# Kernel tuning notes

Measured on AMD Instinct MI355X. Metric: run time of the kernel, lower is better.

Reference implementation:

```python
import math
import jax, jax.numpy as jnp
import numpy as np

B = 128          # graphs per batch
N = 1024         # nodes per graph
E = 1048576      # total edges (avg degree 8)
F_IN = 64
NHID = 64
NCLS = 10
RATIO = 0.8


def setup_inputs() -> dict:
    key = jax.random.key(0)
    ks = jax.random.split(key, 24)
    x = jax.random.normal(ks[0], (B * N, F_IN), jnp.float32)
    # intra-graph random edges: graph id per edge, local src/dst
    epg = E // B
    gid = jnp.repeat(jnp.arange(B, dtype=jnp.int32), epg)
    src = gid * N + jax.random.randint(ks[1], (E,), 0, N, jnp.int32)
    dst = gid * N + jax.random.randint(ks[2], (E,), 0, N, jnp.int32)
    def lin(k, fi, fo):
        s = 1.0 / np.sqrt(fi)
        return jax.random.uniform(k, (fi, fo), jnp.float32, -s, s)
    p = {
        'W1': lin(ks[3], F_IN, NHID), 'b1': jnp.zeros((NHID,), jnp.float32),
        'Wp1': lin(ks[4], NHID, 1), 'bp1': jnp.zeros((1,), jnp.float32),
        'W2': lin(ks[5], NHID, NHID), 'b2': jnp.zeros((NHID,), jnp.float32),
        'Wp2': lin(ks[6], NHID, 1), 'bp2': jnp.zeros((1,), jnp.float32),
        'W3': lin(ks[7], NHID, NHID), 'b3': jnp.zeros((NHID,), jnp.float32),
        'Wp3': lin(ks[8], NHID, 1), 'bp3': jnp.zeros((1,), jnp.float32),
        'L1w': lin(ks[9], 2 * NHID, NHID), 'L1b': jnp.zeros((NHID,), jnp.float32),
        'L2w': lin(ks[10], NHID, NHID // 2), 'L2b': jnp.zeros((NHID // 2,), jnp.float32),
        'L3w': lin(ks[11], NHID // 2, NCLS), 'L3b': jnp.zeros((NCLS,), jnp.float32),
    }
    return dict(x=x, edge_src=src, edge_dst=dst, **p)


def gcn_conv(x, W, b, src, dst, emask, n):
    # PyG GCNConv: add self loops, symmetric deg normalization
    xw = x @ W
    ew = emask.astype(x.dtype)
    deg = jax.ops.segment_sum(ew, dst, num_segments=n) + 1.0  # +1 self loop
    dis = jax.lax.rsqrt(deg)
    norm = dis[src] * dis[dst] * ew
    agg = jax.ops.segment_sum(xw[src] * norm[:, None], dst, num_segments=n)
    agg = agg + xw * (dis * dis)[:, None]  # self-loop message
    return agg + b


def sag_pool(x, Wp, bp, src, dst, emask, n_cur):
    n_tot = B * n_cur
    k = int(math.ceil(RATIO * n_cur))
    score = gcn_conv(x, Wp, bp, src, dst, emask, n_tot)[:, 0]
    _, idx = jax.lax.top_k(score.reshape(B, n_cur), k)
    perm = (idx + (jnp.arange(B, dtype=jnp.int32) * n_cur)[:, None]).reshape(-1)
    xn = x[perm] * jnp.tanh(score[perm])[:, None]
    new_idx = jnp.full((n_tot,), -1, jnp.int32).at[perm].set(
        jnp.arange(B * k, dtype=jnp.int32))
    ns, nd = new_idx[src], new_idx[dst]
    valid = emask & (ns >= 0) & (nd >= 0)
    return xn, jnp.where(valid, ns, 0), jnp.where(valid, nd, 0), valid, k


def readout(x, k):
    xr = x.reshape(B, k, NHID)
    return jnp.concatenate([xr.max(axis=1), xr.mean(axis=1)], axis=1)


def reference(x, edge_src, edge_dst, W1, b1, Wp1, bp1, W2, b2, Wp2, bp2,
              W3, b3, Wp3, bp3, L1w, L1b, L2w, L2b, L3w, L3b):
    src = edge_src.astype(jnp.int32)
    dst = edge_dst.astype(jnp.int32)
    emask = jnp.ones((E,), bool)
    n = N
    h = jax.nn.relu(gcn_conv(x, W1, b1, src, dst, emask, B * n))
    h, src, dst, emask, n = sag_pool(h, Wp1, bp1, src, dst, emask, n)
    r1 = readout(h, n)
    h = jax.nn.relu(gcn_conv(h, W2, b2, src, dst, emask, B * n))
    h, src, dst, emask, n = sag_pool(h, Wp2, bp2, src, dst, emask, n)
    r2 = readout(h, n)
    h = jax.nn.relu(gcn_conv(h, W3, b3, src, dst, emask, B * n))
    h, src, dst, emask, n = sag_pool(h, Wp3, bp3, src, dst, emask, n)
    r3 = readout(h, n)
    z = r1 + r2 + r3
    z = jax.nn.relu(z @ L1w + L1b)          # dropout is identity in eval
    z = jax.nn.relu(z @ L2w + L2b)
    return jax.nn.log_softmax(z @ L3w + L3b, axis=-1)
```

## Files before the change

kernel.cpp:

```cpp
#include <hip/hip_runtime.h>
#include <math.h>

constexpr int B_   = 128;
constexpr int N_   = 1024;
constexpr int E_   = 1048576;
constexpr int BN_  = B_ * N_;
constexpr int EPG  = E_ / B_;
constexpr int SRT2 = EPG + 3 * 1024;
constexpr int NSEG = 16;

typedef short v8s __attribute__((ext_vector_type(8)));
typedef float v4f __attribute__((ext_vector_type(4)));

__device__ __forceinline__ unsigned bf16_rne(unsigned u) {
    return (u + 0x7FFFu + ((u >> 16) & 1u)) >> 16;
}

__global__ __launch_bounds__(1024) void k_csr2(
        const int* __restrict__ src, const int* __restrict__ dst,
        const int* __restrict__ cum,
        int* __restrict__ srt, int* __restrict__ rowptr,
        float* __restrict__ dis, int n) {
    __shared__ int cnt[1024];
    __shared__ int cur[1024];
    __shared__ int cums[1024];
    __shared__ int wsum[17];
    int g = blockIdx.x, tid = threadIdx.x;
    int gb   = g * N_;
    int base = g * n;
    const int eb = g * EPG;
    int* gsrt = srt + (size_t)g * SRT2;

    cums[tid] = cum ? cum[gb + tid] : tid;
    cnt[tid] = 0;
    __syncthreads();
    for (int t = tid; t < EPG; t += 1024) {
        int s = cums[src[eb + t] - gb];
        int d = cums[dst[eb + t] - gb];
        if ((s | d) >= 0) atomicAdd(&cnt[d], 1);
    }
    __syncthreads();

    int c  = (tid < n) ? cnt[tid] : 0;
    int pc = (c + 3) & ~3;
    int v = pc;
    int lane = tid & 63, wv = tid >> 6;
    #pragma unroll
    for (int off = 1; off < 64; off <<= 1) {
        int t = __shfl_up(v, off, 64);
        if (lane >= off) v += t;
    }
    if (lane == 63) wsum[wv] = v;
    __syncthreads();
    if (tid == 0) {
        int run = 0;
        #pragma unroll
        for (int i = 0; i < 16; ++i) { int t = wsum[i]; wsum[i] = run; run += t; }
        wsum[16] = run;
    }
    __syncthreads();
    int excl = v - pc + wsum[wv];
    if (tid < n) {
        cur[tid] = excl;
        rowptr[g * (n + 1) + tid] = excl;
        dis[base + tid] = rsqrtf((float)c + 1.0f);
    }
    if (tid == 0) rowptr[g * (n + 1) + n] = wsum[16];
    __syncthreads();

    for (int t = tid; t < EPG; t += 1024) {
        int s = cums[src[eb + t] - gb];
        int d = cums[dst[eb + t] - gb];
        if ((s | d) < 0) continue;
        int pos = atomicAdd(&cur[d], 1);
        gsrt[pos] = s;
    }
    __syncthreads();

    if (tid < n) {
        int e1 = excl + pc;
        for (int t = cur[tid]; t < e1; ++t) gsrt[t] = n;
    }
}

__global__ __launch_bounds__(1024) void k_wprep3(
        const float* __restrict__ W0, const float* __restrict__ W1,
        const float* __restrict__ W2, unsigned short* __restrict__ wfall) {
    const float* W = (blockIdx.x == 0) ? W0 : (blockIdx.x == 1) ? W1 : W2;
    unsigned short* wf = wfall + (size_t)blockIdx.x * 8192;
    int t = threadIdx.x;
    int l  = t & 63;
    int kk = (t >> 6) & 1;
    int c  = (t >> 7) & 3;
    int p  = (t >> 9) & 1;
    int col = c * 16 + (l & 15);
    int kbase = kk * 32 + (l >> 4) * 8;
    unsigned short o[8];
    #pragma unroll
    for (int j = 0; j < 8; ++j) {
        float w = W[(kbase + j) * 64 + col];
        unsigned u  = __float_as_uint(w);
        unsigned hi = bf16_rne(u);
        if (p == 0) o[j] = (unsigned short)hi;
        else {
            float lo = w - __uint_as_float(hi << 16);
            o[j] = (unsigned short)bf16_rne(__float_as_uint(lo));
        }
    }
    uint4 v;
    v.x = o[0] | ((unsigned)o[1] << 16);
    v.y = o[2] | ((unsigned)o[3] << 16);
    v.z = o[4] | ((unsigned)o[5] << 16);
    v.w = o[6] | ((unsigned)o[7] << 16);
    *reinterpret_cast<uint4*>(wf + (size_t)t * 8) = v;
}

__global__ __launch_bounds__(256) void k_xw_mfma(
        const float* __restrict__ h, const int* __restrict__ perm,
        const float* __restrict__ ggate, const unsigned short* __restrict__ wf,
        const float* __restrict__ dis, float* __restrict__ xwq, int rows) {
    __shared__ float hs[128][68];
    __shared__ float sdis[128];
    __shared__ int   lperm[128];
    __shared__ float lgate[128];
    int tid = threadIdx.x;
    int r0 = blockIdx.x * 128;

    if (perm) {
        if (tid < 128) { lperm[tid] = perm[r0 + tid]; lgate[tid] = ggate[r0 + tid]; }
        __syncthreads();
        for (int i = tid; i < 128 * 16; i += 256) {
            int row = i >> 4, s = i & 15;
            float4 v = *reinterpret_cast<const float4*>(h + (size_t)lperm[row] * 64 + s * 4);
            float gt = lgate[row];
            v.x *= gt; v.y *= gt; v.z *= gt; v.w *= gt;
            *reinterpret_cast<float4*>(&hs[row][s * 4]) = v;
        }
    } else {
        for (int i = tid; i < 128 * 16; i += 256) {
            int row = i >> 4, s = i & 15;
            float4 v = *reinterpret_cast<const float4*>(h + (size_t)(r0 + row) * 64 + s * 4);
            *reinterpret_cast<float4*>(&hs[row][s * 4]) = v;
        }
    }
    if (tid < 128) sdis[tid] = dis[r0 + tid];

    int lane = tid & 63;
    v8s wh[4][2], wl[4][2];
    #pragma unroll
    for (int c = 0; c < 4; ++c) {
        #pragma unroll
        for (int kk = 0; kk < 2; ++kk) {
            wh[c][kk] = *reinterpret_cast<const v8s*>(wf + (((size_t)((0*4 + c)*2 + kk))*64 + lane)*8);
            wl[c][kk] = *reinterpret_cast<const v8s*>(wf + (((size_t)((1*4 + c)*2 + kk))*64 + lane)*8);
        }
    }
    __syncthreads();

    int wave = tid >> 6;
    int m = lane & 15, b = lane >> 4;
    #pragma unroll
    for (int t = 0; t < 2; ++t) {
        int lr0 = (wave * 2 + t) * 16;
        float f[16];
        *reinterpret_cast<float4*>(f)      = *reinterpret_cast<const float4*>(&hs[lr0 + m][b * 8]);
        *reinterpret_cast<float4*>(f + 4)  = *reinterpret_cast<const float4*>(&hs[lr0 + m][b * 8 + 4]);
        *reinterpret_cast<float4*>(f + 8)  = *reinterpret_cast<const float4*>(&hs[lr0 + m][32 + b * 8]);
        *reinterpret_cast<float4*>(f + 12) = *reinterpret_cast<const float4*>(&hs[lr0 + m][32 + b * 8 + 4]);
        v8s ah[2], al[2];
        #pragma unroll
        for (int ch = 0; ch < 2; ++ch) {
            #pragma unroll
            for (int j = 0; j < 8; ++j) {
                float x = f[ch * 8 + j];
                unsigned u  = __float_as_uint(x);
                unsigned hi = bf16_rne(u);
                float lo = x - __uint_as_float(hi << 16);
                ah[ch][j] = (short)hi;
                al[ch][j] = (short)bf16_rne(__float_as_uint(lo));
            }
        }
        float dv[4];
        #pragma unroll
        for (int reg = 0; reg < 4; ++reg) dv[reg] = sdis[lr0 + b * 4 + reg];

        #pragma unroll
        for (int c = 0; c < 4; ++c) {
            v4f acc = {0.f, 0.f, 0.f, 0.f};
            acc = __builtin_amdgcn_mfma_f32_16x16x32_bf16(ah[0], wh[c][0], acc, 0, 0, 0);
            acc = __builtin_amdgcn_mfma_f32_16x16x32_bf16(ah[1], wh[c][1], acc, 0, 0, 0);
            acc = __builtin_amdgcn_mfma_f32_16x16x32_bf16(al[0], wh[c][0], acc, 0, 0, 0);
            acc = __builtin_amdgcn_mfma_f32_16x16x32_bf16(al[1], wh[c][1], acc, 0, 0, 0);
            acc = __builtin_amdgcn_mfma_f32_16x16x32_bf16(ah[0], wl[c][0], acc, 0, 0, 0);
            acc = __builtin_amdgcn_mfma_f32_16x16x32_bf16(ah[1], wl[c][1], acc, 0, 0, 0);
            acc = __builtin_amdgcn_mfma_f32_16x16x32_bf16(al[0], wl[c][0], acc, 0, 0, 0);
            acc = __builtin_amdgcn_mfma_f32_16x16x32_bf16(al[1], wl[c][1], acc, 0, 0, 0);
            #pragma unroll
            for (int reg = 0; reg < 4; ++reg) {
                int grow = r0 + lr0 + b * 4 + reg;
                xwq[((size_t)c * rows + grow) * 16 + m] = acc[reg] * dv[reg];
            }
        }
    }
}

__global__ __launch_bounds__(1024, 8) void k_agg8(
        const int* __restrict__ srt, const int* __restrict__ rowptr,
        const float* __restrict__ dis, const float* __restrict__ xwq,
        const float* __restrict__ bias, const float* __restrict__ Wp,
        float* __restrict__ hout, float* __restrict__ sagg8,
        int n, int rows) {
    extern __shared__ float xs[];
    int lrpPad = (n + 4) & ~3;
    int* lrp = (int*)(xs + (n + 1) * 12);
    unsigned short* lsrtU = (unsigned short*)(lrp + lrpPad);

    int g = blockIdx.x & 127, e8 = blockIdx.x >> 7;
    int q = e8 >> 1, half = (e8 & 1) * 8;
    int foff = q * 16 + half;
    int tid  = threadIdx.x;
    int base = g * n;
    const float* plane = xwq + ((size_t)q * rows + base) * 16 + half;

    for (int i = tid; i < n * 2; i += 1024) {
        int row = i >> 1, s = i & 1;
        float4 v = *reinterpret_cast<const float4*>(plane + row * 16 + s * 4);
        *reinterpret_cast<float4*>(xs + row * 12 + s * 4) = v;
    }
    if (tid < 12) xs[n * 12 + tid] = 0.0f;
    for (int i = tid; i <= n; i += 1024) lrp[i] = rowptr[g * (n + 1) + i];
    __syncthreads();
    int total = lrp[n];
    const int* gsrt = srt + (size_t)g * SRT2;
    for (int i = tid; i < total; i += 1024) lsrtU[i] = (unsigned short)gsrt[i];
    __syncthreads();

    int sub = tid & 1;
    float4 bq  = *reinterpret_cast<const float4*>(bias + foff + sub * 4);
    float4 wp4 = *reinterpret_cast<const float4*>(Wp   + foff + sub * 4);
    for (int row = tid >> 1; row < n; row += 512) {
        int s0 = lrp[row], s1 = lrp[row + 1];
        float4 acc = *reinterpret_cast<const float4*>(xs + row * 12 + sub * 4);
        for (int j = s0; j < s1; j += 4) {
            ushort4 nb = *reinterpret_cast<const ushort4*>(lsrtU + j);
            const float4 v0 = *reinterpret_cast<const float4*>(xs + nb.x * 12 + sub * 4);
            const float4 v1 = *reinterpret_cast<const float4*>(xs + nb.y * 12 + sub * 4);
            const float4 v2 = *reinterpret_cast<const float4*>(xs + nb.z * 12 + sub * 4);
            const float4 v3 = *reinterpret_cast<const float4*>(xs + nb.w * 12 + sub * 4);
            acc.x += v0.x + v1.x + v2.x + v3.x;
            acc.y += v0.y + v1.y + v2.y + v3.y;
            acc.z += v0.z + v1.z + v2.z + v3.z;
            acc.w += v0.w + v1.w + v2.w + v3.w;
        }
        float dsc = dis[base + row];
        float4 o;
        o.x = fmaxf(fmaf(dsc, acc.x, bq.x), 0.0f);
        o.y = fmaxf(fmaf(dsc, acc.y, bq.y), 0.0f);
        o.z = fmaxf(fmaf(dsc, acc.z, bq.z), 0.0f);
        o.w = fmaxf(fmaf(dsc, acc.w, bq.w), 0.0f);
        *reinterpret_cast<float4*>(hout + (size_t)(base + row) * 64 + foff + sub * 4) = o;
        float part = o.x * wp4.x + o.y * wp4.y + o.z * wp4.z + o.w * wp4.w;
        part += __shfl_xor(part, 1, 64);
        if (sub == 0) xs[row * 12 + 8] = part * dsc;
    }
    __syncthreads();

    for (int row = tid; row < n; row += 1024) {
        float acc = xs[row * 12 + 8];
        int s1 = lrp[row + 1];
        for (int j = lrp[row]; j < s1; j += 4) {
            ushort4 nb = *reinterpret_cast<const ushort4*>(lsrtU + j);
            acc += xs[nb.x * 12 + 8] + xs[nb.y * 12 + 8]
                 + xs[nb.z * 12 + 8] + xs[nb.w * 12 + 8];
        }
        sagg8[(size_t)e8 * BN_ + base + row] = acc;
    }
}

__global__ __launch_bounds__(1024) void k_score_topk(
        const float* __restrict__ dis, const float* __restrict__ sagg8,
        const float* __restrict__ bp, int n, int k,
        int* __restrict__ perm, float* __restrict__ ggate,
        int* __restrict__ cum, int do_compose) {
    __shared__ unsigned long long keys[1024];
    __shared__ int mark[1024];
    int g = blockIdx.x, tid = threadIdx.x;
    int base = g * n;
    float bp0 = bp[0];

    unsigned long long kv = 0ull;
    if (tid < n) {
        float s0 = 0.0f;
        #pragma unroll
        for (int p = 0; p < 8; ++p) s0 += sagg8[(size_t)p * BN_ + base + tid];
        float sag = dis[base + tid] * s0 + bp0;
        unsigned u  = __float_as_uint(sag);
        unsigned mk = (u & 0x80000000u) ? ~u : (u | 0x80000000u);
        kv = ((unsigned long long)mk << 32) | (unsigned)tid;
    }
    keys[tid] = kv;
    mark[tid] = -1;

    for (int size = 2; size <= 1024; size <<= 1) {
        for (int stride = size >> 1; stride > 0; stride >>= 1) {
            __syncthreads();
            if (tid < 512) {
                int a  = ((tid / stride) * (stride << 1)) + (tid & (stride - 1));
                int bx = a + stride;
                bool asc = ((a & size) == 0);
                unsigned long long ka = keys[a], kb = keys[bx];
                bool sw = asc ? (ka > kb) : (ka < kb);
                if (sw) { keys[a] = kb; keys[bx] = ka; }
            }
        }
    }
    __syncthreads();

    if (tid < k) {
        int j = tid;
        unsigned long long kvv = keys[1023 - j];
        int local   = (int)(kvv & 0xFFFFFFFFull);
        unsigned mk = (unsigned)(kvv >> 32);
        unsigned u  = (mk & 0x80000000u) ? (mk ^ 0x80000000u) : ~mk;
        int newg = g * k + j;
        perm[newg]  = base + local;
        ggate[newg] = tanhf(__uint_as_float(u));
        mark[local] = j;
    }
    __syncthreads();
    if (do_compose) {
        int gb = g * N_;
        int c = (do_compose == 1) ? tid : cum[gb + tid];
        cum[gb + tid] = (c >= 0) ? mark[c] : -1;
    }
}

__global__ __launch_bounds__(256) void k_readout_seg(
        const float* __restrict__ h, const int* __restrict__ perm,
        const float* __restrict__ ggate, int k, float* __restrict__ pz) {
    int g = blockIdx.x / NSEG, seg = blockIdx.x % NSEG;
    int ck = (k + NSEG - 1) / NSEG;
    int j0 = seg * ck;
    int j1 = min(k, j0 + ck);
    __shared__ float gate[64];
    __shared__ int   lperm[64];
    int tid = threadIdx.x;
    for (int j = j0 + tid; j < j1; j += 256) {
        lperm[j - j0] = perm[g * k + j];
        gate[j - j0]  = ggate[g * k + j];
    }
    __syncthreads();
    int lane = tid & 63, w = tid >> 6;
    float mx = -INFINITY, sm = 0.0f;
    for (int j = j0 + w; j < j1; j += 4) {
        float v = h[(size_t)lperm[j - j0] * 64 + lane] * gate[j - j0];
        mx = fmaxf(mx, v); sm += v;
    }
    __shared__ float smx[4][64], ssm[4][64];
    smx[w][lane] = mx; ssm[w][lane] = sm;
    __syncthreads();
    if (w == 0) {
        #pragma unroll
        for (int i = 1; i < 4; ++i) { mx = fmaxf(mx, smx[i][lane]); sm += ssm[i][lane]; }
        float* p = pz + ((size_t)g * NSEG + seg) * 128;
        p[lane]      = mx;
        p[64 + lane] = sm;
    }
}

__global__ __launch_bounds__(128) void k_mlp(const float* __restrict__ pz,
                      const float* __restrict__ L1w, const float* __restrict__ L1b,
                      const float* __restrict__ L2w, const float* __restrict__ L2b,
                      const float* __restrict__ L3w, const float* __restrict__ L3b,
                      float* __restrict__ out) {
    __shared__ float z[128], h1[64], h2[32], lg[10], lse;
    int g = blockIdx.x, tid = threadIdx.x;
    const float kinv[3] = {1.0f / 820.0f, 1.0f / 656.0f, 1.0f / 525.0f};
    float zv = 0.0f;
    if (tid < 64) {
        #pragma unroll
        for (int L = 0; L < 3; ++L) {
            const float* p = pz + (((size_t)L * B_ + g) * NSEG) * 128;
            float mx = -INFINITY;
            #pragma unroll
            for (int s = 0; s < NSEG; ++s) mx = fmaxf(mx, p[s * 128 + tid]);
            zv += mx;
        }
    } else {
        int f = tid - 64;
        #pragma unroll
        for (int L = 0; L < 3; ++L) {
            const float* p = pz + (((size_t)L * B_ + g) * NSEG) * 128;
            float sm = 0.0f;
            #pragma unroll
            for (int s = 0; s < NSEG; ++s) sm += p[s * 128 + 64 + f];
            zv += sm * kinv[L];
        }
    }
    z[tid] = zv;
    __syncthreads();
    if (tid < 64) {
        float acc = L1b[tid];
        for (int i = 0; i < 128; ++i) acc = fmaf(z[i], L1w[i * 64 + tid], acc);
        h1[tid] = fmaxf(acc, 0.0f);
    }
    __syncthreads();
    if (tid < 32) {
        float acc = L2b[tid];
        for (int i = 0; i < 64; ++i) acc = fmaf(h1[i], L2w[i * 32 + tid], acc);
        h2[tid] = fmaxf(acc, 0.0f);
    }
    __syncthreads();
    if (tid < 10) {
        float acc = L3b[tid];
        for (int i = 0; i < 32; ++i) acc = fmaf(h2[i], L3w[i * 10 + tid], acc);
        lg[tid] = acc;
    }
    __syncthreads();
    if (tid == 0) {
        float m = lg[0];
        for (int i = 1; i < 10; ++i) m = fmaxf(m, lg[i]);
        float s = 0.0f;
        for (int i = 0; i < 10; ++i) s += expf(lg[i] - m);
        lse = m + logf(s);
    }
    __syncthreads();
    if (tid < 10) out[g * 10 + tid] = lg[tid] - lse;
}

extern "C" void kernel_launch(void* const* d_in, const int* in_sizes, int n_in,
                              void* d_out, int out_size, void* d_ws, size_t ws_size,
                              hipStream_t stream) {
    const float* x    = (const float*)d_in[0];
    const int*   esrc = (const int*)d_in[1];
    const int*   edst = (const int*)d_in[2];
    const float* W [3] = {(const float*)d_in[3],  (const float*)d_in[7],  (const float*)d_in[11]};
    const float* bb[3] = {(const float*)d_in[4],  (const float*)d_in[8],  (const float*)d_in[12]};
    const float* Wp[3] = {(const float*)d_in[5],  (const float*)d_in[9],  (const float*)d_in[13]};
    const float* bp[3] = {(const float*)d_in[6],  (const float*)d_in[10], (const float*)d_in[14]};
    const float* L1w = (const float*)d_in[15];
    const float* L1b = (const float*)d_in[16];
    const float* L2w = (const float*)d_in[17];
    const float* L2b = (const float*)d_in[18];
    const float* L3w = (const float*)d_in[19];
    const float* L3b = (const float*)d_in[20];
    float* out = (float*)d_out;

    float* fws   = (float*)d_ws;
    float* agg   = fws;
    float* xwq   = agg  + (size_t)BN_ * 64;
    float* dis   = xwq  + (size_t)BN_ * 64;
    float* sagg8 = dis  + BN_;
    float* ggate = sagg8 + 8 * (size_t)BN_;
    float* pz    = ggate + BN_;
    int*   perm   = (int*)(pz + 3 * B_ * NSEG * 128);
    int*   cum    = perm + BN_;
    int*   srt    = cum + BN_;
    int*   rowptr = srt + (size_t)B_ * SRT2;
    unsigned short* wfrag = (unsigned short*)(rowptr + B_ * (N_ + 1));

    hipFuncSetAttribute(reinterpret_cast<const void*>(k_agg8),
                        hipFuncAttributeMaxDynamicSharedMemorySize,
                        1025 * 12 * 4 + 1028 * 4 + SRT2 * 2);

    k_wprep3<<<3, 1024, 0, stream>>>(W[0], W[1], W[2], wfrag);

    const int ks_[3] = {820, 656, 525};
    int n = N_;

    for (int L = 0; L < 3; ++L) {
        int rows = B_ * n;
        int k    = ks_[L];

        k_csr2<<<B_, 1024, 0, stream>>>(esrc, edst, (L == 0) ? nullptr : cum,
                                        srt, rowptr, dis, n);

        if (L == 0)
            k_xw_mfma<<<rows / 128, 256, 0, stream>>>(x, nullptr, nullptr,
                                                      wfrag, dis, xwq, rows);
        else
            k_xw_mfma<<<rows / 128, 256, 0, stream>>>(agg, perm, ggate,
                                                      wfrag + (size_t)L * 8192, dis, xwq, rows);

        int lrpPad = (n + 4) & ~3;
        size_t ldsB = (size_t)(n + 1) * 12 * 4 + (size_t)lrpPad * 4 + (size_t)SRT2 * 2;
        k_agg8<<<B_ * 8, 1024, ldsB, stream>>>(
            srt, rowptr, dis, xwq, bb[L], Wp[L], agg, sagg8, n, rows);

        k_score_topk<<<B_, 1024, 0, stream>>>(dis, sagg8, bp[L], n, k,
                                              perm, ggate, cum, (L < 2) ? (L + 1) : 0);

        k_readout_seg<<<B_ * NSEG, 256, 0, stream>>>(agg, perm, ggate, k,
                                                     pz + (size_t)L * B_ * NSEG * 128);

        n = k;
    }

    k_mlp<<<B_, 128, 0, stream>>>(pz, L1w, L1b, L2w, L2b, L3w, L3b, out);
}
```

Measured before the change: 264.6 us.

## Replace LDS-staged feature-plane aggregation with wave-per-row global gather

Drops the 8-way feature-split aggregation kernel, which staged a graph's feature plane and CSR into LDS. Each wave now owns a run of rows and gathers full 64-wide rows from a row-major xw buffer in global memory, one lane per feature. The CSR no longer pads rows to multiples of 4, and neighbour reduction of the SAG score is moved into the top-k kernel, which works from a single per-node partial score instead of 8 partial planes. This removes the LDS staging and padding work but relies on uncached global gathers with serial per-edge loop latency and fewer, larger blocks.

New measurement: 351.6 us. 1.33x slower.

```diff
diff --git a/kernel.cpp b/kernel.cpp
--- a/kernel.cpp
+++ b/kernel.cpp
@@ -6,7 +6,6 @@
 constexpr int E_   = 1048576;
 constexpr int BN_  = B_ * N_;
 constexpr int EPG  = E_ / B_;
-constexpr int SRT2 = EPG + 3 * 1024;
 constexpr int NSEG = 16;
 
 typedef short v8s __attribute__((ext_vector_type(8)));
@@ -29,7 +28,6 @@
     int gb   = g * N_;
     int base = g * n;
     const int eb = g * EPG;
-    int* gsrt = srt + (size_t)g * SRT2;
 
     cums[tid] = cum ? cum[gb + tid] : tid;
     cnt[tid] = 0;
@@ -41,9 +39,8 @@
     }
     __syncthreads();
 
-    int c  = (tid < n) ? cnt[tid] : 0;
-    int pc = (c + 3) & ~3;
-    int v = pc;
+    int c = (tid < n) ? cnt[tid] : 0;
+    int v = c;
     int lane = tid & 63, wv = tid >> 6;
     #pragma unroll
     for (int off = 1; off < 64; off <<= 1) {
@@ -59,7 +56,7 @@
         wsum[16] = run;
     }
     __syncthreads();
-    int excl = v - pc + wsum[wv];
+    int excl = v - c + wsum[wv];
     if (tid < n) {
         cur[tid] = excl;
         rowptr[g * (n + 1) + tid] = excl;
@@ -73,13 +70,7 @@
         int d = cums[dst[eb + t] - gb];
         if ((s | d) < 0) continue;
         int pos = atomicAdd(&cur[d], 1);
-        gsrt[pos] = s;
-    }
-    __syncthreads();
-
-    if (tid < n) {
-        int e1 = excl + pc;
-        for (int t = cur[tid]; t < e1; ++t) gsrt[t] = n;
+        srt[eb + pos] = s;
     }
 }
 
@@ -118,7 +109,7 @@
 __global__ __launch_bounds__(256) void k_xw_mfma(
         const float* __restrict__ h, const int* __restrict__ perm,
         const float* __restrict__ ggate, const unsigned short* __restrict__ wf,
-        const float* __restrict__ dis, float* __restrict__ xwq, int rows) {
+        const float* __restrict__ dis, float* __restrict__ xw, int rows) {
     __shared__ float hs[128][68];
     __shared__ float sdis[128];
     __shared__ int   lperm[128];
@@ -198,102 +189,72 @@
             #pragma unroll
             for (int reg = 0; reg < 4; ++reg) {
                 int grow = r0 + lr0 + b * 4 + reg;
-                xwq[((size_t)c * rows + grow) * 16 + m] = acc[reg] * dv[reg];
+                xw[(size_t)grow * 64 + c * 16 + m] = acc[reg] * dv[reg];
             }
         }
     }
 }
 
-__global__ __launch_bounds__(1024, 8) void k_agg8(
+__global__ __launch_bounds__(1024) void k_agg_gather(
         const int* __restrict__ srt, const int* __restrict__ rowptr,
-        const float* __restrict__ dis, const float* __restrict__ xwq,
+        const float* __restrict__ dis, const float* __restrict__ xw,
         const float* __restrict__ bias, const float* __restrict__ Wp,
-        float* __restrict__ hout, float* __restrict__ sagg8,
-        int n, int rows) {
-    extern __shared__ float xs[];
-    int lrpPad = (n + 4) & ~3;
-    int* lrp = (int*)(xs + (n + 1) * 12);
-    unsigned short* lsrtU = (unsigned short*)(lrp + lrpPad);
-
-    int g = blockIdx.x & 127, e8 = blockIdx.x >> 7;
-    int q = e8 >> 1, half = (e8 & 1) * 8;
-    int foff = q * 16 + half;
-    int tid  = threadIdx.x;
+        float* __restrict__ hout, float* __restrict__ ps, int n) {
+    int g = blockIdx.x & 127, quarter = blockIdx.x >> 7;
+    int tid = threadIdx.x, lane = tid & 63, wave = tid >> 6;
     int base = g * n;
-    const float* plane = xwq + ((size_t)q * rows + base) * 16 + half;
-
-    for (int i = tid; i < n * 2; i += 1024) {
-        int row = i >> 1, s = i & 1;
-        float4 v = *reinterpret_cast<const float4*>(plane + row * 16 + s * 4);
-        *reinterpret_cast<float4*>(xs + row * 12 + s * 4) = v;
-    }
-    if (tid < 12) xs[n * 12 + tid] = 0.0f;
-    for (int i = tid; i <= n; i += 1024) lrp[i] = rowptr[g * (n + 1) + i];
-    __syncthreads();
-    int total = lrp[n];
-    const int* gsrt = srt + (size_t)g * SRT2;
-    for (int i = tid; i < total; i += 1024) lsrtU[i] = (unsigned short)gsrt[i];
-    __syncthreads();
-
-    int sub = tid & 1;
-    float4 bq  = *reinterpret_cast<const float4*>(bias + foff + sub * 4);
-    float4 wp4 = *reinterpret_cast<const float4*>(Wp   + foff + sub * 4);
-    for (int row = tid >> 1; row < n; row += 512) {
-        int s0 = lrp[row], s1 = lrp[row + 1];
-        float4 acc = *reinterpret_cast<const float4*>(xs + row * 12 + sub * 4);
-        for (int j = s0; j < s1; j += 4) {
-            ushort4 nb = *reinterpret_cast<const ushort4*>(lsrtU + j);
-            const float4 v0 = *reinterpret_cast<const float4*>(xs + nb.x * 12 + sub * 4);
-            const float4 v1 = *reinterpret_cast<const float4*>(xs + nb.y * 12 + sub * 4);
-            const float4 v2 = *reinterpret_cast<const float4*>(xs + nb.z * 12 + sub * 4);
-            const float4 v3 = *reinterpret_cast<const float4*>(xs + nb.w * 12 + sub * 4);
-            acc.x += v0.x + v1.x + v2.x + v3.x;
-            acc.y += v0.y + v1.y + v2.y + v3.y;
-            acc.z += v0.z + v1.z + v2.z + v3.z;
-            acc.w += v0.w + v1.w + v2.w + v3.w;
-        }
-        float dsc = dis[base + row];
-        float4 o;
-        o.x = fmaxf(fmaf(dsc, acc.x, bq.x), 0.0f);
-        o.y = fmaxf(fmaf(dsc, acc.y, bq.y), 0.0f);
-        o.z = fmaxf(fmaf(dsc, acc.z, bq.z), 0.0f);
-        o.w = fmaxf(fmaf(dsc, acc.w, bq.w), 0.0f);
-        *reinterpret_cast<float4*>(hout + (size_t)(base + row) * 64 + foff + sub * 4) = o;
-        float part = o.x * wp4.x + o.y * wp4.y + o.z * wp4.z + o.w * wp4.w;
-        part += __shfl_xor(part, 1, 64);
-        if (sub == 0) xs[row * 12 + 8] = part * dsc;
-    }
-    __syncthreads();
-
-    for (int row = tid; row < n; row += 1024) {
-        float acc = xs[row * 12 + 8];
-        int s1 = lrp[row + 1];
-        for (int j = lrp[row]; j < s1; j += 4) {
-            ushort4 nb = *reinterpret_cast<const ushort4*>(lsrtU + j);
-            acc += xs[nb.x * 12 + 8] + xs[nb.y * 12 + 8]
-                 + xs[nb.z * 12 + 8] + xs[nb.w * 12 + 8];
-        }
-        sagg8[(size_t)e8 * BN_ + base + row] = acc;
+    int nq  = (n + 3) >> 2;
+    int rpw = (nq + 15) >> 4;
+    int r0 = quarter * nq + wave * rpw;
+    int r1 = min(min(r0 + rpw, (quarter + 1) * nq), n);
+
+    float bq  = bias[lane];
+    float wpl = Wp[lane];
+    const float* xg  = xw + (size_t)base * 64;
+    const int* gsrt  = srt + g * EPG;
+    const int* grp   = rowptr + g * (n + 1);
+
+    for (int r = r0; r < r1; ++r) {
+        int s0 = grp[r], s1 = grp[r + 1];
+        float acc = xg[(size_t)r * 64 + lane];
+        for (int j = s0; j < s1; ++j) {
+            int src = gsrt[j];
+            acc += xg[(size_t)src * 64 + lane];
+        }
+        float dsc = dis[base + r];
+        float o = fmaxf(fmaf(dsc, acc, bq), 0.0f);
+        hout[(size_t)(base + r) * 64 + lane] = o;
+        float part = o * wpl;
+        #pragma unroll
+        for (int off = 32; off; off >>= 1) part += __shfl_xor(part, off, 64);
+        if (lane == 0) ps[base + r] = part * dsc;
     }
 }
 
 __global__ __launch_bounds__(1024) void k_score_topk(
-        const float* __restrict__ dis, const float* __restrict__ sagg8,
+        const int* __restrict__ srt, const int* __restrict__ rowptr,
+        const float* __restrict__ dis, const float* __restrict__ ps,
         const float* __restrict__ bp, int n, int k,
         int* __restrict__ perm, float* __restrict__ ggate,
         int* __restrict__ cum, int do_compose) {
+    __shared__ float psl[1024];
     __shared__ unsigned long long keys[1024];
     __shared__ int mark[1024];
     int g = blockIdx.x, tid = threadIdx.x;
     int base = g * n;
     float bp0 = bp[0];
+    const int* gsrt = srt + g * EPG;
+    const int* grp  = rowptr + g * (n + 1);
+
+    psl[tid] = (tid < n) ? ps[base + tid] : 0.0f;
+    __syncthreads();
 
     unsigned long long kv = 0ull;
     if (tid < n) {
-        float s0 = 0.0f;
-        #pragma unroll
-        for (int p = 0; p < 8; ++p) s0 += sagg8[(size_t)p * BN_ + base + tid];
-        float sag = dis[base + tid] * s0 + bp0;
+        float acc = psl[tid];
+        int s1 = grp[tid + 1];
+        for (int j = grp[tid]; j < s1; ++j) acc += psl[gsrt[j]];
+        float sag = dis[base + tid] * acc + bp0;
         unsigned u  = __float_as_uint(sag);
         unsigned mk = (u & 0x80000000u) ? ~u : (u | 0x80000000u);
         kv = ((unsigned long long)mk << 32) | (unsigned)tid;
@@ -448,20 +409,16 @@
 
     float* fws   = (float*)d_ws;
     float* agg   = fws;
-    float* xwq   = agg  + (size_t)BN_ * 64;
-    float* dis   = xwq  + (size_t)BN_ * 64;
-    float* sagg8 = dis  + BN_;
-    float* ggate = sagg8 + 8 * (size_t)BN_;
+    float* xw    = agg  + (size_t)BN_ * 64;
+    float* dis   = xw   + (size_t)BN_ * 64;
+    float* ps    = dis  + BN_;
+    float* ggate = ps   + BN_;
     float* pz    = ggate + BN_;
     int*   perm   = (int*)(pz + 3 * B_ * NSEG * 128);
     int*   cum    = perm + BN_;
     int*   srt    = cum + BN_;
-    int*   rowptr = srt + (size_t)B_ * SRT2;
+    int*   rowptr = srt + E_;
     unsigned short* wfrag = (unsigned short*)(rowptr + B_ * (N_ + 1));
-
-    hipFuncSetAttribute(reinterpret_cast<const void*>(k_agg8),
-                        hipFuncAttributeMaxDynamicSharedMemorySize,
-                        1025 * 12 * 4 + 1028 * 4 + SRT2 * 2);
 
     k_wprep3<<<3, 1024, 0, stream>>>(W[0], W[1], W[2], wfrag);
 
@@ -477,17 +434,15 @@
 
         if (L == 0)
             k_xw_mfma<<<rows / 128, 256, 0, stream>>>(x, nullptr, nullptr,
-                                                      wfrag, dis, xwq, rows);
+                                                      wfrag, dis, xw, rows);
         else
             k_xw_mfma<<<rows / 128, 256, 0, stream>>>(agg, perm, ggate,
-                                                      wfrag + (size_t)L * 8192, dis, xwq, rows);
-
-        int lrpPad = (n + 4) & ~3;
-        size_t ldsB = (size_t)(n + 1) * 12 * 4 + (size_t)lrpPad * 4 + (size_t)SRT2 * 2;
-        k_agg8<<<B_ * 8, 1024, ldsB, stream>>>(
-            srt, rowptr, dis, xwq, bb[L], Wp[L], agg, sagg8, n, rows);
-
-        k_score_topk<<<B_, 1024, 0, stream>>>(dis, sagg8, bp[L], n, k,
+                                                      wfrag + (size_t)L * 8192, dis, xw, rows);
+
+        k_agg_gather<<<B_ * 4, 1024, 0, stream>>>(
+            srt, rowptr, dis, xw, bb[L], Wp[L], agg, ps, n);
+
+        k_score_topk<<<B_, 1024, 0, stream>>>(srt, rowptr, dis, ps, bp[L], n, k,
                                               perm, ggate, cum, (L < 2) ? (L + 1) : 0);
 
         k_readout_seg<<<B_ * NSEG, 256, 0, stream>>>(agg, perm, ggate, k,
```
